# Optimization experiments

Hardware: AMD Instinct MI355X
Metric: run time of the kernel (lower is better)

The kernel has to match this reference:

```python
import jax, jax.numpy as jnp
import numpy as np

ONE_WAY = False  # init kwarg: if False, messages flow both directions along each bond

def setup_inputs() -> dict:
    key = jax.random.key(0)
    k1, k2, k3, k4 = jax.random.split(key, 4)
    B, N, D, E = 32, 2048, 256, 1 << 20
    x = jax.random.normal(k1, (B, N, D), dtype=jnp.float32)
    batch_idx = jax.random.randint(k2, (E,), 0, B, dtype=jnp.int64)
    src_idx = jax.random.randint(k3, (E,), 0, N, dtype=jnp.int64)
    dst_idx = jax.random.randint(k4, (E,), 0, N, dtype=jnp.int64)
    return {"x": x, "batch_idx": batch_idx, "src_idx": src_idx, "dst_idx": dst_idx}

def reference(x, batch_idx, src_idx, dst_idx):
    B, N, D = x.shape
    x_flat = x.reshape(B * N, D)
    # flatten (batch, node) -> single segment id so one scatter-add covers all edges
    src = batch_idx * N + src_idx
    dst = batch_idx * N + dst_idx
    out = jnp.zeros_like(x_flat).at[dst].add(x_flat[src])
    if not ONE_WAY:
        out = out.at[src].add(x_flat[dst])
    out = out.reshape(B, N, D)
    return jnp.concatenate([out, x], axis=2)  # [B, N, 2D]
```

## Files before the change

kernel.cpp:

```cpp
#include <hip/hip_runtime.h>

#define NB   32
#define NN   2048
#define RTOT (NB * NN)
#define DIM  256
#define DIM2 512
#define CAP  128

#define EPT    4
#define NPASS  8
#define PSHIFT 13
#define CONV_BLOCKS   512
#define CONV_PER_BLK  (RTOT * DIM / 4 / CONV_BLOCKS)

#define BLKS_PER_BATCH (NN / 4)
#define GATHER_BLOCKS  (RTOT / 4)


typedef float vf4 __attribute__((ext_vector_type(4)));
typedef unsigned short vu4 __attribute__((ext_vector_type(4)));

__global__ __launch_bounds__(256) void zero_counts(int* __restrict__ c) {
    int i = blockIdx.x * 256 + threadIdx.x;
    if (i < RTOT) c[i] = 0;
}

__device__ inline vf4 bf16x4_to_f32(unsigned lo, unsigned hi) {
    vf4 v;
    v[0] = __uint_as_float(lo << 16);
    v[1] = __uint_as_float(lo & 0xffff0000u);
    v[2] = __uint_as_float(hi << 16);
    v[3] = __uint_as_float(hi & 0xffff0000u);
    return v;
}

__global__ __launch_bounds__(256) void fill_conv(const int* __restrict__ b,
                                                 const int* __restrict__ s,
                                                 const int* __restrict__ d,
                                                 int* __restrict__ cnt,
                                                 unsigned short* __restrict__ bucket,
                                                 const float* __restrict__ x,
                                                 unsigned short* __restrict__ xb,
                                                 int E, int fillBlocks) {
    if ((int)blockIdx.x >= fillBlocks) {
        int cb = blockIdx.x - fillBlocks;
        const vf4* x4 = (const vf4*)x;
        vu4* o4 = (vu4*)xb;
        int beg = cb * CONV_PER_BLK;
        for (int i = beg + (int)threadIdx.x; i < beg + CONV_PER_BLK; i += 256) {
            vf4 v = x4[i];
            vu4 o;
#pragma unroll
            for (int k = 0; k < 4; ++k) {
                unsigned u = __float_as_uint(v[k]);
                unsigned r = u + 0x7fffu + ((u >> 16) & 1u);
                o[k] = (unsigned short)(r >> 16);
            }
            o4[i] = o;
        }
        return;
    }

    int t = blockIdx.x * 256 + threadIdx.x;
    int base = t * EPT;

    int rs[EPT], rd[EPT];

    if (base + EPT <= E) {
        int4 b4 = ((const int4*)b)[t];
        int4 s4 = ((const int4*)s)[t];
        int4 d4 = ((const int4*)d)[t];
        rs[0] = b4.x * NN + s4.x;  rd[0] = b4.x * NN + d4.x;
        rs[1] = b4.y * NN + s4.y;  rd[1] = b4.y * NN + d4.y;
        rs[2] = b4.z * NN + s4.z;  rd[2] = b4.z * NN + d4.z;
        rs[3] = b4.w * NN + s4.w;  rd[3] = b4.w * NN + d4.w;
    } else {
#pragma unroll
        for (int i = 0; i < EPT; ++i) {
            int e = base + i;
            if (e < E) {
                int bb = b[e];
                rs[i] = bb * NN + s[e];
                rd[i] = bb * NN + d[e];
            } else {
                rs[i] = -1;
                rd[i] = -1;
            }
        }
    }

    for (int p = 0; p < NPASS; ++p) {
#pragma unroll
        for (int i = 0; i < EPT; ++i) {
            if ((rs[i] >> PSHIFT) == p) {
                int q = atomicAdd(&cnt[rs[i]], 1);
                if (q < CAP) bucket[(long)rs[i] * CAP + q] = (unsigned short)rd[i];
            }
            if ((rd[i] >> PSHIFT) == p) {
                int q = atomicAdd(&cnt[rd[i]], 1);
                if (q < CAP) bucket[(long)rd[i] * CAP + q] = (unsigned short)rs[i];
            }
        }
    }
}

__global__ __launch_bounds__(256) void gather_bf16(const float* __restrict__ x,
                                                   const unsigned short* __restrict__ xb,
                                                   const int* __restrict__ cnt,
                                                   const unsigned short* __restrict__ bucket,
                                                   float* __restrict__ out) {
    int p = blockIdx.x;
    int l;
    if (gridDim.x == GATHER_BLOCKS) {
        int xcd = p & 7;
        int u   = p >> 3;
        int bat = xcd + 8 * (u >> 9);
        l = bat * BLKS_PER_BATCH + (u & (BLKS_PER_BATCH - 1));
    } else {
        l = p;
    }

    int lane = threadIdx.x & 63;
    int half = lane >> 5;
    int sub  = lane & 31;
    int row = __builtin_amdgcn_readfirstlane((l << 2) + (threadIdx.x >> 6));
    if (row >= RTOT) return;

    int n = __builtin_amdgcn_readfirstlane(cnt[row]);
    if (n > CAP) n = CAP;
    const unsigned* l32 = (const unsigned*)(bucket + (size_t)row * CAP);

    const uint4* xb4 = (const uint4*)xb;
    const vf4*   x4  = (const vf4*)x;
    vf4 xown = x4[((size_t)row << 6) + lane];

    vf4 aA0 = (vf4){0.f,0.f,0.f,0.f};
    vf4 aB0 = (vf4){0.f,0.f,0.f,0.f};
    vf4 aA1 = (vf4){0.f,0.f,0.f,0.f};
    vf4 aB1 = (vf4){0.f,0.f,0.f,0.f};

    int pairs = n >> 1;
    int j = 0;
    for (; j + 4 <= pairs; j += 4) {
        unsigned w0 = l32[j + 0];
        unsigned w1 = l32[j + 1];
        unsigned w2 = l32[j + 2];
        unsigned w3 = l32[j + 3];
        unsigned r0 = half ? (w0 >> 16) : (w0 & 0xffffu);
        unsigned r1 = half ? (w1 >> 16) : (w1 & 0xffffu);
        unsigned r2 = half ? (w2 >> 16) : (w2 & 0xffffu);
        unsigned r3 = half ? (w3 >> 16) : (w3 & 0xffffu);
        uint4 q0 = xb4[(size_t)((r0 << 5) + sub)];
        uint4 q1 = xb4[(size_t)((r1 << 5) + sub)];
        uint4 q2 = xb4[(size_t)((r2 << 5) + sub)];
        uint4 q3 = xb4[(size_t)((r3 << 5) + sub)];
        aA0 += bf16x4_to_f32(q0.x, q0.y); aB0 += bf16x4_to_f32(q0.z, q0.w);
        aA1 += bf16x4_to_f32(q1.x, q1.y); aB1 += bf16x4_to_f32(q1.z, q1.w);
        aA0 += bf16x4_to_f32(q2.x, q2.y); aB0 += bf16x4_to_f32(q2.z, q2.w);
        aA1 += bf16x4_to_f32(q3.x, q3.y); aB1 += bf16x4_to_f32(q3.z, q3.w);
    }
    for (; j < pairs; ++j) {
        unsigned w0 = l32[j];
        unsigned r0 = half ? (w0 >> 16) : (w0 & 0xffffu);
        uint4 q0 = xb4[(size_t)((r0 << 5) + sub)];
        aA0 += bf16x4_to_f32(q0.x, q0.y); aB0 += bf16x4_to_f32(q0.z, q0.w);
    }
    if (n & 1) {
        unsigned w0 = l32[pairs];
        unsigned r0 = w0 & 0xffffu;
        if (half == 0) {
            uint4 q0 = xb4[(size_t)((r0 << 5) + sub)];
            aA0 += bf16x4_to_f32(q0.x, q0.y); aB0 += bf16x4_to_f32(q0.z, q0.w);
        }
    }

    vf4 aA = aA0 + aA1;
    vf4 aB = aB0 + aB1;
#pragma unroll
    for (int k = 0; k < 4; ++k) {
        aA[k] += __shfl_xor(aA[k], 32, 64);
        aB[k] += __shfl_xor(aB[k], 32, 64);
    }

    vf4* o = (vf4*)(out + (size_t)row * DIM2);
    if (half == 0) {
        __builtin_nontemporal_store(aA, &o[2 * sub]);
        __builtin_nontemporal_store(aB, &o[2 * sub + 1]);
    }
    __builtin_nontemporal_store(xown, &o[64 + lane]);
}

__global__ __launch_bounds__(256) void gather_f32(const float* __restrict__ x,
                                                  const int* __restrict__ cnt,
                                                  const unsigned short* __restrict__ bucket,
                                                  float* __restrict__ out) {
    int p = blockIdx.x;
    int l;
    if (gridDim.x == GATHER_BLOCKS) {
        int xcd = p & 7;
        int u   = p >> 3;
        int bat = xcd + 8 * (u >> 9);
        l = bat * BLKS_PER_BATCH + (u & (BLKS_PER_BATCH - 1));
    } else {
        l = p;
    }
    int lane = threadIdx.x & 63;
    int row = __builtin_amdgcn_readfirstlane((l << 2) + (threadIdx.x >> 6));
    if (row >= RTOT) return;
    int n = __builtin_amdgcn_readfirstlane(cnt[row]);
    if (n > CAP) n = CAP;
    const unsigned* l32 = (const unsigned*)(bucket + (size_t)row * CAP);
    const vf4* x4 = (const vf4*)x;
    vf4 xown = x4[((size_t)row << 6) + lane];
    vf4 acc0 = (vf4){0.f,0.f,0.f,0.f};
    vf4 acc1 = (vf4){0.f,0.f,0.f,0.f};
    vf4 acc2 = (vf4){0.f,0.f,0.f,0.f};
    vf4 acc3 = (vf4){0.f,0.f,0.f,0.f};
    int j = 0;
    for (; j + 8 <= n; j += 8) {
        int k = j >> 1;
        unsigned w0 = l32[k+0], w1 = l32[k+1], w2 = l32[k+2], w3 = l32[k+3];
        unsigned r0 = w0 & 0xffffu, r1 = w0 >> 16;
        unsigned r2 = w1 & 0xffffu, r3 = w1 >> 16;
        unsigned r4 = w2 & 0xffffu, r5 = w2 >> 16;
        unsigned r6 = w3 & 0xffffu, r7 = w3 >> 16;
        vf4 a0 = x4[(size_t)((r0 << 6) + lane)];
        vf4 a1 = x4[(size_t)((r1 << 6) + lane)];
        vf4 a2 = x4[(size_t)((r2 << 6) + lane)];
        vf4 a3 = x4[(size_t)((r3 << 6) + lane)];
        vf4 a4 = x4[(size_t)((r4 << 6) + lane)];
        vf4 a5 = x4[(size_t)((r5 << 6) + lane)];
        vf4 a6 = x4[(size_t)((r6 << 6) + lane)];
        vf4 a7 = x4[(size_t)((r7 << 6) + lane)];
        acc0 += a0; acc1 += a1; acc2 += a2; acc3 += a3;
        acc0 += a4; acc1 += a5; acc2 += a6; acc3 += a7;
    }
    for (; j + 4 <= n; j += 4) {
        int k = j >> 1;
        unsigned w0 = l32[k+0], w1 = l32[k+1];
        unsigned r0 = w0 & 0xffffu, r1 = w0 >> 16;
        unsigned r2 = w1 & 0xffffu, r3 = w1 >> 16;
        vf4 a0 = x4[(size_t)((r0 << 6) + lane)];
        vf4 a1 = x4[(size_t)((r1 << 6) + lane)];
        vf4 a2 = x4[(size_t)((r2 << 6) + lane)];
        vf4 a3 = x4[(size_t)((r3 << 6) + lane)];
        acc0 += a0; acc1 += a1; acc2 += a2; acc3 += a3;
    }
    for (; j < n; ++j) {
        unsigned w0 = l32[j >> 1];
        unsigned r = (j & 1) ? (w0 >> 16) : (w0 & 0xffffu);
        acc0 += x4[(size_t)((r << 6) + lane)];
    }
    vf4 acc = (acc0 + acc1) + (acc2 + acc3);
    vf4* o = (vf4*)(out + (size_t)row * DIM2);
    __builtin_nontemporal_store(acc,  &o[lane]);
    __builtin_nontemporal_store(xown, &o[64 + lane]);
}

extern "C" void kernel_launch(void* const* d_in, const int* in_sizes, int n_in,
                              void* d_out, int out_size, void* d_ws, size_t ws_size,
                              hipStream_t stream) {
    const float* x         = (const float*)d_in[0];
    const int*   batch_idx = (const int*)d_in[1];
    const int*   src_idx   = (const int*)d_in[2];
    const int*   dst_idx   = (const int*)d_in[3];
    float*       out       = (float*)d_out;

    const int E = in_sizes[1];

    int* cnt = (int*)d_ws;
    unsigned short* bucket = (unsigned short*)(cnt + RTOT);
    unsigned short* xb = bucket + (size_t)RTOT * CAP;
    size_t need = (size_t)RTOT * 4 + (size_t)RTOT * CAP * 2 + (size_t)RTOT * DIM * 2;
    bool use_bf16 = (ws_size >= need);

    zero_counts<<<(RTOT + 255) / 256, 256, 0, stream>>>(cnt);

    int threads_needed = (E + EPT - 1) / EPT;
    int fillBlocks = (threads_needed + 255) / 256;
    int grid = fillBlocks + (use_bf16 ? CONV_BLOCKS : 0);
    fill_conv<<<grid, 256, 0, stream>>>(batch_idx, src_idx, dst_idx,
                                        cnt, bucket, x, xb, E, fillBlocks);

    if (use_bf16) {
        gather_bf16<<<GATHER_BLOCKS, 256, 0, stream>>>(x, xb, cnt, bucket, out);
    } else {
        gather_f32<<<GATHER_BLOCKS, 256, 0, stream>>>(x, cnt, bucket, out);
    }
}
```

Measured before the change: 296.8 us.

## Privatize bucket counters into eight copies to cut atomic contention

Adds a path that splits each row's counter and bucket into eight private copies, chosen by fill-block index, each holding up to 32 entries. The goal is to spread atomic contention on the per-row counters across more addresses. The gather kernel now reads eight counts per row and walks the eight segments in an interleaved loop with per-segment predicates. This costs eight times the counter zeroing, a bucket region twice as large, and more divergent control in gather. The fp32 fallback is removed, so when the workspace is too small for the new layout the code now runs the bf16 path without checking that it fits.

```diff
diff --git a/kernel.cpp b/kernel.cpp
--- a/kernel.cpp
+++ b/kernel.cpp
@@ -6,6 +6,7 @@
 #define DIM  256
 #define DIM2 512
 #define CAP  128
+#define CAPX 32
 
 #define EPT    4
 #define NPASS  8
@@ -20,9 +21,9 @@
 typedef float vf4 __attribute__((ext_vector_type(4)));
 typedef unsigned short vu4 __attribute__((ext_vector_type(4)));
 
-__global__ __launch_bounds__(256) void zero_counts(int* __restrict__ c) {
+__global__ __launch_bounds__(256) void zero_counts(int* __restrict__ c, int n) {
     int i = blockIdx.x * 256 + threadIdx.x;
-    if (i < RTOT) c[i] = 0;
+    if (i < n) c[i] = 0;
 }
 
 __device__ inline vf4 bf16x4_to_f32(unsigned lo, unsigned hi) {
@@ -32,6 +33,185 @@
     v[2] = __uint_as_float(hi << 16);
     v[3] = __uint_as_float(hi & 0xffff0000u);
     return v;
+}
+
+__device__ inline void conv_path(const float* __restrict__ x,
+                                 unsigned short* __restrict__ xb, int cb) {
+    const vf4* x4 = (const vf4*)x;
+    vu4* o4 = (vu4*)xb;
+    int beg = cb * CONV_PER_BLK;
+    for (int i = beg + (int)threadIdx.x; i < beg + CONV_PER_BLK; i += 256) {
+        vf4 v = x4[i];
+        vu4 o;
+#pragma unroll
+        for (int k = 0; k < 4; ++k) {
+            unsigned u = __float_as_uint(v[k]);
+            unsigned r = u + 0x7fffu + ((u >> 16) & 1u);
+            o[k] = (unsigned short)(r >> 16);
+        }
+        o4[i] = o;
+    }
+}
+
+__global__ __launch_bounds__(256) void fill_conv_priv(const int* __restrict__ b,
+                                                      const int* __restrict__ s,
+                                                      const int* __restrict__ d,
+                                                      int* __restrict__ cnt8,
+                                                      unsigned short* __restrict__ bucket,
+                                                      const float* __restrict__ x,
+                                                      unsigned short* __restrict__ xb,
+                                                      int E, int fillBlocks) {
+    if ((int)blockIdx.x >= fillBlocks) {
+        conv_path(x, xb, blockIdx.x - fillBlocks);
+        return;
+    }
+    int kcopy = blockIdx.x & 7;
+    int* cnt = cnt8 + kcopy * RTOT;
+    int koff = kcopy * CAPX;
+
+    int t = blockIdx.x * 256 + threadIdx.x;
+    int base = t * EPT;
+    int rs[EPT], rd[EPT];
+
+    if (base + EPT <= E) {
+        int4 b4 = ((const int4*)b)[t];
+        int4 s4 = ((const int4*)s)[t];
+        int4 d4 = ((const int4*)d)[t];
+        rs[0] = b4.x * NN + s4.x;  rd[0] = b4.x * NN + d4.x;
+        rs[1] = b4.y * NN + s4.y;  rd[1] = b4.y * NN + d4.y;
+        rs[2] = b4.z * NN + s4.z;  rd[2] = b4.z * NN + d4.z;
+        rs[3] = b4.w * NN + s4.w;  rd[3] = b4.w * NN + d4.w;
+    } else {
+#pragma unroll
+        for (int i = 0; i < EPT; ++i) {
+            int e = base + i;
+            if (e < E) {
+                int bb = b[e];
+                rs[i] = bb * NN + s[e];
+                rd[i] = bb * NN + d[e];
+            } else { rs[i] = -1; rd[i] = -1; }
+        }
+    }
+
+    for (int p = 0; p < NPASS; ++p) {
+#pragma unroll
+        for (int i = 0; i < EPT; ++i) {
+            if ((rs[i] >> PSHIFT) == p) {
+                int q = atomicAdd(&cnt[rs[i]], 1);
+                if (q < CAPX) bucket[(long)rs[i] * 256 + koff + q] = (unsigned short)rd[i];
+            }
+            if ((rd[i] >> PSHIFT) == p) {
+                int q = atomicAdd(&cnt[rd[i]], 1);
+                if (q < CAPX) bucket[(long)rd[i] * 256 + koff + q] = (unsigned short)rs[i];
+            }
+        }
+    }
+}
+
+__global__ __launch_bounds__(256) void gather_priv(const float* __restrict__ x,
+                                                   const unsigned short* __restrict__ xb,
+                                                   const int* __restrict__ cnt8,
+                                                   const unsigned short* __restrict__ bucket,
+                                                   float* __restrict__ out) {
+    int p = blockIdx.x;
+    int l;
+    if (gridDim.x == GATHER_BLOCKS) {
+        int xcd = p & 7;
+        int u   = p >> 3;
+        int bat = xcd + 8 * (u >> 9);
+        l = bat * BLKS_PER_BATCH + (u & (BLKS_PER_BATCH - 1));
+    } else {
+        l = p;
+    }
+
+    int lane = threadIdx.x & 63;
+    int half = lane >> 5;
+    int sub  = lane & 31;
+    int row = __builtin_amdgcn_readfirstlane((l << 2) + (threadIdx.x >> 6));
+    if (row >= RTOT) return;
+
+    int n0 = __builtin_amdgcn_readfirstlane(cnt8[0 * RTOT + row]); if (n0 > CAPX) n0 = CAPX;
+    int n1 = __builtin_amdgcn_readfirstlane(cnt8[1 * RTOT + row]); if (n1 > CAPX) n1 = CAPX;
+    int n2 = __builtin_amdgcn_readfirstlane(cnt8[2 * RTOT + row]); if (n2 > CAPX) n2 = CAPX;
+    int n3 = __builtin_amdgcn_readfirstlane(cnt8[3 * RTOT + row]); if (n3 > CAPX) n3 = CAPX;
+    int n4 = __builtin_amdgcn_readfirstlane(cnt8[4 * RTOT + row]); if (n4 > CAPX) n4 = CAPX;
+    int n5 = __builtin_amdgcn_readfirstlane(cnt8[5 * RTOT + row]); if (n5 > CAPX) n5 = CAPX;
+    int n6 = __builtin_amdgcn_readfirstlane(cnt8[6 * RTOT + row]); if (n6 > CAPX) n6 = CAPX;
+    int n7 = __builtin_amdgcn_readfirstlane(cnt8[7 * RTOT + row]); if (n7 > CAPX) n7 = CAPX;
+
+    const unsigned* l32 = (const unsigned*)(bucket + (size_t)row * 256);
+    const uint4* xb4 = (const uint4*)xb;
+    const vf4*   x4  = (const vf4*)x;
+    vf4 xown = x4[((size_t)row << 6) + lane];
+
+    vf4 aA0 = (vf4){0.f,0.f,0.f,0.f};
+    vf4 aB0 = (vf4){0.f,0.f,0.f,0.f};
+    vf4 aA1 = (vf4){0.f,0.f,0.f,0.f};
+    vf4 aB1 = (vf4){0.f,0.f,0.f,0.f};
+
+    int p0 = n0 >> 1, p1 = n1 >> 1, p2 = n2 >> 1, p3 = n3 >> 1;
+    int p4 = n4 >> 1, p5 = n5 >> 1, p6 = n6 >> 1, p7 = n7 >> 1;
+    int maxp = p0;
+    if (p1 > maxp) maxp = p1;  if (p2 > maxp) maxp = p2;
+    if (p3 > maxp) maxp = p3;  if (p4 > maxp) maxp = p4;
+    if (p5 > maxp) maxp = p5;  if (p6 > maxp) maxp = p6;
+    if (p7 > maxp) maxp = p7;
+
+#define SEG_LOAD(K, PK, Q)                                             \
+    uint4 Q;                                                           \
+    if (i < (PK)) {                                                    \
+        unsigned w_ = l32[(K) * 16 + i];                               \
+        unsigned r_ = half ? (w_ >> 16) : (w_ & 0xffffu);              \
+        Q = xb4[(size_t)((r_ << 5) + sub)];                            \
+    }
+#define SEG_ACC(PK, Q, AA, BB)                                         \
+    if (i < (PK)) {                                                    \
+        (AA) += bf16x4_to_f32((Q).x, (Q).y);                           \
+        (BB) += bf16x4_to_f32((Q).z, (Q).w);                           \
+    }
+
+    for (int i = 0; i < maxp; ++i) {
+        SEG_LOAD(0, p0, q0) SEG_LOAD(1, p1, q1)
+        SEG_LOAD(2, p2, q2) SEG_LOAD(3, p3, q3)
+        SEG_LOAD(4, p4, q4) SEG_LOAD(5, p5, q5)
+        SEG_LOAD(6, p6, q6) SEG_LOAD(7, p7, q7)
+        SEG_ACC(p0, q0, aA0, aB0) SEG_ACC(p1, q1, aA1, aB1)
+        SEG_ACC(p2, q2, aA0, aB0) SEG_ACC(p3, q3, aA1, aB1)
+        SEG_ACC(p4, q4, aA0, aB0) SEG_ACC(p5, q5, aA1, aB1)
+        SEG_ACC(p6, q6, aA0, aB0) SEG_ACC(p7, q7, aA1, aB1)
+    }
+#undef SEG_LOAD
+#undef SEG_ACC
+
+#define SEG_ODD(K, NK, PK)                                             \
+    if ((NK) & 1) {                                                    \
+        unsigned w_ = l32[(K) * 16 + (PK)];                            \
+        if (half == 0) {                                               \
+            unsigned r_ = w_ & 0xffffu;                                \
+            uint4 q_ = xb4[(size_t)((r_ << 5) + sub)];                 \
+            aA0 += bf16x4_to_f32(q_.x, q_.y);                          \
+            aB0 += bf16x4_to_f32(q_.z, q_.w);                          \
+        }                                                              \
+    }
+    SEG_ODD(0, n0, p0) SEG_ODD(1, n1, p1) SEG_ODD(2, n2, p2)
+    SEG_ODD(3, n3, p3) SEG_ODD(4, n4, p4) SEG_ODD(5, n5, p5)
+    SEG_ODD(6, n6, p6) SEG_ODD(7, n7, p7)
+#undef SEG_ODD
+
+    vf4 aA = aA0 + aA1;
+    vf4 aB = aB0 + aB1;
+#pragma unroll
+    for (int k = 0; k < 4; ++k) {
+        aA[k] += __shfl_xor(aA[k], 32, 64);
+        aB[k] += __shfl_xor(aB[k], 32, 64);
+    }
+
+    vf4* o = (vf4*)(out + (size_t)row * DIM2);
+    if (half == 0) {
+        __builtin_nontemporal_store(aA, &o[2 * sub]);
+        __builtin_nontemporal_store(aB, &o[2 * sub + 1]);
+    }
+    __builtin_nontemporal_store(xown, &o[64 + lane]);
 }
 
 __global__ __launch_bounds__(256) void fill_conv(const int* __restrict__ b,
@@ -43,29 +223,12 @@
                                                  unsigned short* __restrict__ xb,
                                                  int E, int fillBlocks) {
     if ((int)blockIdx.x >= fillBlocks) {
-        int cb = blockIdx.x - fillBlocks;
-        const vf4* x4 = (const vf4*)x;
-        vu4* o4 = (vu4*)xb;
-        int beg = cb * CONV_PER_BLK;
-        for (int i = beg + (int)threadIdx.x; i < beg + CONV_PER_BLK; i += 256) {
-            vf4 v = x4[i];
-            vu4 o;
-#pragma unroll
-            for (int k = 0; k < 4; ++k) {
-                unsigned u = __float_as_uint(v[k]);
-                unsigned r = u + 0x7fffu + ((u >> 16) & 1u);
-                o[k] = (unsigned short)(r >> 16);
-            }
-            o4[i] = o;
-        }
+        conv_path(x, xb, blockIdx.x - fillBlocks);
         return;
     }
-
     int t = blockIdx.x * 256 + threadIdx.x;
     int base = t * EPT;
-
     int rs[EPT], rd[EPT];
-
     if (base + EPT <= E) {
         int4 b4 = ((const int4*)b)[t];
         int4 s4 = ((const int4*)s)[t];
@@ -82,13 +245,9 @@
                 int bb = b[e];
                 rs[i] = bb * NN + s[e];
                 rd[i] = bb * NN + d[e];
-            } else {
-                rs[i] = -1;
-                rd[i] = -1;
-            }
-        }
-    }
-
+            } else { rs[i] = -1; rd[i] = -1; }
+        }
+    }
     for (int p = 0; p < NPASS; ++p) {
 #pragma unroll
         for (int i = 0; i < EPT; ++i) {
@@ -119,33 +278,25 @@
     } else {
         l = p;
     }
-
     int lane = threadIdx.x & 63;
     int half = lane >> 5;
     int sub  = lane & 31;
     int row = __builtin_amdgcn_readfirstlane((l << 2) + (threadIdx.x >> 6));
     if (row >= RTOT) return;
-
     int n = __builtin_amdgcn_readfirstlane(cnt[row]);
     if (n > CAP) n = CAP;
     const unsigned* l32 = (const unsigned*)(bucket + (size_t)row * CAP);
-
     const uint4* xb4 = (const uint4*)xb;
     const vf4*   x4  = (const vf4*)x;
     vf4 xown = x4[((size_t)row << 6) + lane];
-
     vf4 aA0 = (vf4){0.f,0.f,0.f,0.f};
     vf4 aB0 = (vf4){0.f,0.f,0.f,0.f};
     vf4 aA1 = (vf4){0.f,0.f,0.f,0.f};
     vf4 aB1 = (vf4){0.f,0.f,0.f,0.f};
-
     int pairs = n >> 1;
     int j = 0;
     for (; j + 4 <= pairs; j += 4) {
-        unsigned w0 = l32[j + 0];
-        unsigned w1 = l32[j + 1];
-        unsigned w2 = l32[j + 2];
-        unsigned w3 = l32[j + 3];
+        unsigned w0 = l32[j + 0], w1 = l32[j + 1], w2 = l32[j + 2], w3 = l32[j + 3];
         unsigned r0 = half ? (w0 >> 16) : (w0 & 0xffffu);
         unsigned r1 = half ? (w1 >> 16) : (w1 & 0xffffu);
         unsigned r2 = half ? (w2 >> 16) : (w2 & 0xffffu);
@@ -173,7 +324,6 @@
             aA0 += bf16x4_to_f32(q0.x, q0.y); aB0 += bf16x4_to_f32(q0.z, q0.w);
         }
     }
-
     vf4 aA = aA0 + aA1;
     vf4 aB = aB0 + aB1;
 #pragma unroll
@@ -181,79 +331,11 @@
         aA[k] += __shfl_xor(aA[k], 32, 64);
         aB[k] += __shfl_xor(aB[k], 32, 64);
     }
-
     vf4* o = (vf4*)(out + (size_t)row * DIM2);
     if (half == 0) {
         __builtin_nontemporal_store(aA, &o[2 * sub]);
         __builtin_nontemporal_store(aB, &o[2 * sub + 1]);
     }
-    __builtin_nontemporal_store(xown, &o[64 + lane]);
-}
-
-__global__ __launch_bounds__(256) void gather_f32(const float* __restrict__ x,
-                                                  const int* __restrict__ cnt,
-                                                  const unsigned short* __restrict__ bucket,
-                                                  float* __restrict__ out) {
-    int p = blockIdx.x;
-    int l;
-    if (gridDim.x == GATHER_BLOCKS) {
-        int xcd = p & 7;
-        int u   = p >> 3;
-        int bat = xcd + 8 * (u >> 9);
-        l = bat * BLKS_PER_BATCH + (u & (BLKS_PER_BATCH - 1));
-    } else {
-        l = p;
-    }
-    int lane = threadIdx.x & 63;
-    int row = __builtin_amdgcn_readfirstlane((l << 2) + (threadIdx.x >> 6));
-    if (row >= RTOT) return;
-    int n = __builtin_amdgcn_readfirstlane(cnt[row]);
-    if (n > CAP) n = CAP;
-    const unsigned* l32 = (const unsigned*)(bucket + (size_t)row * CAP);
-    const vf4* x4 = (const vf4*)x;
-    vf4 xown = x4[((size_t)row << 6) + lane];
-    vf4 acc0 = (vf4){0.f,0.f,0.f,0.f};
-    vf4 acc1 = (vf4){0.f,0.f,0.f,0.f};
-    vf4 acc2 = (vf4){0.f,0.f,0.f,0.f};
-    vf4 acc3 = (vf4){0.f,0.f,0.f,0.f};
-    int j = 0;
-    for (; j + 8 <= n; j += 8) {
-        int k = j >> 1;
-        unsigned w0 = l32[k+0], w1 = l32[k+1], w2 = l32[k+2], w3 = l32[k+3];
-        unsigned r0 = w0 & 0xffffu, r1 = w0 >> 16;
-        unsigned r2 = w1 & 0xffffu, r3 = w1 >> 16;
-        unsigned r4 = w2 & 0xffffu, r5 = w2 >> 16;
-        unsigned r6 = w3 & 0xffffu, r7 = w3 >> 16;
-        vf4 a0 = x4[(size_t)((r0 << 6) + lane)];
-        vf4 a1 = x4[(size_t)((r1 << 6) + lane)];
-        vf4 a2 = x4[(size_t)((r2 << 6) + lane)];
-        vf4 a3 = x4[(size_t)((r3 << 6) + lane)];
-        vf4 a4 = x4[(size_t)((r4 << 6) + lane)];
-        vf4 a5 = x4[(size_t)((r5 << 6) + lane)];
-        vf4 a6 = x4[(size_t)((r6 << 6) + lane)];
-        vf4 a7 = x4[(size_t)((r7 << 6) + lane)];
-        acc0 += a0; acc1 += a1; acc2 += a2; acc3 += a3;
-        acc0 += a4; acc1 += a5; acc2 += a6; acc3 += a7;
-    }
-    for (; j + 4 <= n; j += 4) {
-        int k = j >> 1;
-        unsigned w0 = l32[k+0], w1 = l32[k+1];
-        unsigned r0 = w0 & 0xffffu, r1 = w0 >> 16;
-        unsigned r2 = w1 & 0xffffu, r3 = w1 >> 16;
-        vf4 a0 = x4[(size_t)((r0 << 6) + lane)];
-        vf4 a1 = x4[(size_t)((r1 << 6) + lane)];
-        vf4 a2 = x4[(size_t)((r2 << 6) + lane)];
-        vf4 a3 = x4[(size_t)((r3 << 6) + lane)];
-        acc0 += a0; acc1 += a1; acc2 += a2; acc3 += a3;
-    }
-    for (; j < n; ++j) {
-        unsigned w0 = l32[j >> 1];
-        unsigned r = (j & 1) ? (w0 >> 16) : (w0 & 0xffffu);
-        acc0 += x4[(size_t)((r << 6) + lane)];
-    }
-    vf4 acc = (acc0 + acc1) + (acc2 + acc3);
-    vf4* o = (vf4*)(out + (size_t)row * DIM2);
-    __builtin_nontemporal_store(acc,  &o[lane]);
     __builtin_nontemporal_store(xown, &o[64 + lane]);
 }
 
@@ -268,23 +350,30 @@
 
     const int E = in_sizes[1];
 
-    int* cnt = (int*)d_ws;
-    unsigned short* bucket = (unsigned short*)(cnt + RTOT);
-    unsigned short* xb = bucket + (size_t)RTOT * CAP;
-    size_t need = (size_t)RTOT * 4 + (size_t)RTOT * CAP * 2 + (size_t)RTOT * DIM * 2;
-    bool use_bf16 = (ws_size >= need);
-
-    zero_counts<<<(RTOT + 255) / 256, 256, 0, stream>>>(cnt);
-
     int threads_needed = (E + EPT - 1) / EPT;
     int fillBlocks = (threads_needed + 255) / 256;
-    int grid = fillBlocks + (use_bf16 ? CONV_BLOCKS : 0);
-    fill_conv<<<grid, 256, 0, stream>>>(batch_idx, src_idx, dst_idx,
-                                        cnt, bucket, x, xb, E, fillBlocks);
-
-    if (use_bf16) {
+
+    size_t need_priv = (size_t)RTOT * 8 * 4 + (size_t)RTOT * 256 * 2
+                     + (size_t)RTOT * DIM * 2;
+    size_t need_r8 = (size_t)RTOT * 4 + (size_t)RTOT * CAP * 2
+                   + (size_t)RTOT * DIM * 2;
+
+    if (ws_size >= need_priv) {
+        int* cnt8 = (int*)d_ws;
+        unsigned short* bucket = (unsigned short*)(cnt8 + RTOT * 8);
+        unsigned short* xb = bucket + (size_t)RTOT * 256;
+        zero_counts<<<(RTOT * 8 + 255) / 256, 256, 0, stream>>>(cnt8, RTOT * 8);
+        fill_conv_priv<<<fillBlocks + CONV_BLOCKS, 256, 0, stream>>>(
+            batch_idx, src_idx, dst_idx, cnt8, bucket, x, xb, E, fillBlocks);
+        gather_priv<<<GATHER_BLOCKS, 256, 0, stream>>>(x, xb, cnt8, bucket, out);
+    } else {
+        int* cnt = (int*)d_ws;
+        unsigned short* bucket = (unsigned short*)(cnt + RTOT);
+        unsigned short* xb = bucket + (size_t)RTOT * CAP;
+        (void)need_r8;
+        zero_counts<<<(RTOT + 255) / 256, 256, 0, stream>>>(cnt, RTOT);
+        fill_conv<<<fillBlocks + CONV_BLOCKS, 256, 0, stream>>>(
+            batch_idx, src_idx, dst_idx, cnt, bucket, x, xb, E, fillBlocks);
         gather_bf16<<<GATHER_BLOCKS, 256, 0, stream>>>(x, xb, cnt, bucket, out);
-    } else {
-        gather_f32<<<GATHER_BLOCKS, 256, 0, stream>>>(x, cnt, bucket, out);
-    }
-}
+    }
+}
```

After: 360.2 us. 1.21x slower.
